# Optimization experiments

Hardware: AMD Instinct MI355X
Metric: run time of the kernel (lower is better)

The kernel has to match this reference:

```python
import jax, jax.numpy as jnp
import numpy as np

M, IN, H, OUT, B = 64, 64, 256, 1, 4096


def setup_inputs() -> dict:
    key = jax.random.key(0)
    ks = jax.random.split(key, 7)
    s1 = 1.0 / np.sqrt(IN)
    s2 = 1.0 / np.sqrt(H)
    return {
        "xs": jax.random.normal(ks[0], (M, B, IN), dtype=jnp.float32),
        "W1": jax.random.uniform(ks[1], (M, IN, H), minval=-s1, maxval=s1, dtype=jnp.float32),
        "b1": jax.random.uniform(ks[2], (M, H), minval=-s1, maxval=s1, dtype=jnp.float32),
        "W2": jax.random.uniform(ks[3], (M, H, H), minval=-s2, maxval=s2, dtype=jnp.float32),
        "b2": jax.random.uniform(ks[4], (M, H), minval=-s2, maxval=s2, dtype=jnp.float32),
        "W3": jax.random.uniform(ks[5], (M, H, OUT), minval=-s2, maxval=s2, dtype=jnp.float32),
        "b3": jax.random.uniform(ks[6], (M, OUT), minval=-s2, maxval=s2, dtype=jnp.float32),
    }


def reference(xs, W1, b1, W2, b2, W3, b3):
    # Batched over models: [M, B, in] x [M, in, h] -> [M, B, h]
    h1 = jax.nn.relu(jnp.einsum("mbi,mih->mbh", xs, W1) + b1[:, None, :])
    h2 = jax.nn.relu(jnp.einsum("mbh,mhk->mbk", h1, W2) + b2[:, None, :])
    out = jnp.einsum("mbh,mho->mbo", h2, W3) + b3[:, None, :]
    return out  # [M, B, out]
```

## Files before the change

### kernel.cpp

```cpp
#include <hip/hip_runtime.h>

#define NMODELS 64
#define BBATCH  4096
#define IN_DIM  64
#define H_DIM   256

typedef __attribute__((ext_vector_type(8))) short short8;
typedef __attribute__((ext_vector_type(4))) short short4v;
typedef __attribute__((ext_vector_type(4))) float floatx4;

__device__ __forceinline__ unsigned short f2bf(float f) {
    unsigned int u = __builtin_bit_cast(unsigned int, f);
    return (unsigned short)((u + 0x8000u) >> 16);
}

__global__ __launch_bounds__(256) void prep_weights(const float* __restrict__ W1,
                                                    const float* __restrict__ W2,
                                                    unsigned short* __restrict__ w1t,
                                                    unsigned short* __restrict__ w2t) {
    __shared__ float lds[64][65];
    const int bid = blockIdx.x;
    const float* src;
    unsigned short* dst;
    int K, N, m, kb, nb;
    if (bid < 256) {
        m = bid >> 2; kb = 0; nb = bid & 3; K = IN_DIM; N = H_DIM;
        src = W1; dst = w1t;
    } else {
        int t = bid - 256;
        m = t >> 4; kb = (t >> 2) & 3; nb = t & 3; K = H_DIM; N = H_DIM;
        src = W2; dst = w2t;
    }
    const float* s = src + ((size_t)m * K + (size_t)kb * 64) * N + nb * 64;
    const int tid = threadIdx.x;
    const int r = tid >> 4, c4 = (tid & 15) * 4;
#pragma unroll
    for (int p = 0; p < 4; ++p) {
        int row = p * 16 + r;
        float4 v = *(const float4*)(s + (size_t)row * N + c4);
        lds[row][c4] = v.x; lds[row][c4 + 1] = v.y;
        lds[row][c4 + 2] = v.z; lds[row][c4 + 3] = v.w;
    }
    __syncthreads();
    const int n = tid & 63, kg = tid >> 6;
    unsigned short tmp[16];
#pragma unroll
    for (int j = 0; j < 16; ++j) tmp[j] = f2bf(lds[kg * 16 + j][n]);
    unsigned short* d = dst + ((size_t)m * N + (size_t)(nb * 64 + n)) * K + kb * 64 + kg * 16;
    *(short8*)d = *(const short8*)tmp;
    *(short8*)(d + 8) = *(const short8*)(tmp + 8);
}

__global__ __launch_bounds__(256, 4) void mlp_fused(
    const float* __restrict__ xs,
    const unsigned short* __restrict__ w1t,
    const float* __restrict__ b1,
    const unsigned short* __restrict__ w2t,
    const float* __restrict__ b2,
    const float* __restrict__ w3,
    const float* __restrict__ b3,
    float* __restrict__ out)
{
    __shared__ unsigned short h1s[64 * 256];
    float* red = (float*)h1s;

    const int bid = blockIdx.x;
    const int m   = bid >> 6;
    const int tb  = bid & 63;
    const int tid = threadIdx.x;
    const int w   = tid >> 6;
    const int lane = tid & 63;
    const int q   = lane >> 4;
    const int c16 = lane & 15;
    const int sw  = c16 & 7;

    const float* xrow = xs + ((size_t)m * BBATCH + (size_t)tb * 64) * IN_DIM;
    const unsigned short* w1p = w1t + (size_t)m * (H_DIM * IN_DIM)
                                + (w * 64 + c16 * 4) * IN_DIM + q * 8;

    short8 ax[4][2];
#pragma unroll
    for (int rb = 0; rb < 4; ++rb)
#pragma unroll
        for (int kb = 0; kb < 2; ++kb) {
            const float* xp = xrow + (rb * 16 + c16) * IN_DIM + kb * 32 + q * 8;
            float4 v0 = *(const float4*)xp;
            float4 v1 = *(const float4*)(xp + 4);
            short8 a;
            a[0] = (short)f2bf(v0.x); a[1] = (short)f2bf(v0.y);
            a[2] = (short)f2bf(v0.z); a[3] = (short)f2bf(v0.w);
            a[4] = (short)f2bf(v1.x); a[5] = (short)f2bf(v1.y);
            a[6] = (short)f2bf(v1.z); a[7] = (short)f2bf(v1.w);
            ax[rb][kb] = a;
        }

    floatx4 acc[4][4];
#pragma unroll
    for (int rb = 0; rb < 4; ++rb)
#pragma unroll
        for (int nb = 0; nb < 4; ++nb)
            acc[rb][nb] = (floatx4){0.f, 0.f, 0.f, 0.f};

#pragma unroll
    for (int kb = 0; kb < 2; ++kb) {
        short8 bw[4];
#pragma unroll
        for (int nb = 0; nb < 4; ++nb)
            bw[nb] = *(const short8*)(w1p + nb * IN_DIM + kb * 32);
#pragma unroll
        for (int nb = 0; nb < 4; ++nb)
#pragma unroll
            for (int rb = 0; rb < 4; ++rb)
                acc[rb][nb] = __builtin_amdgcn_mfma_f32_16x16x32_bf16(
                    ax[rb][kb], bw[nb], acc[rb][nb], 0, 0, 0);
    }

    {
        floatx4 b1v = *(const floatx4*)(b1 + m * H_DIM + w * 64 + c16 * 4);
#pragma unroll
        for (int rb = 0; rb < 4; ++rb)
#pragma unroll
            for (int r = 0; r < 4; ++r) {
                short4v t;
#pragma unroll
                for (int nb = 0; nb < 4; ++nb)
                    t[nb] = (short)f2bf(fmaxf(acc[rb][nb][r] + b1v[nb], 0.f));
                int row = rb * 16 + q * 4 + r;
                int chunk = (w * 8 + (c16 >> 1)) ^ (row & 7);
                *(short4v*)((char*)h1s + row * 512 + chunk * 16 + (c16 & 1) * 8) = t;
            }
    }
    __syncthreads();

#pragma unroll
    for (int rb = 0; rb < 4; ++rb)
#pragma unroll
        for (int nb = 0; nb < 4; ++nb)
            acc[rb][nb] = (floatx4){0.f, 0.f, 0.f, 0.f};

    const unsigned short* w2p = w2t + (size_t)m * (H_DIM * H_DIM)
                                + (w * 64 + c16 * 4) * H_DIM + q * 8;
#pragma unroll
    for (int kb = 0; kb < 8; ++kb) {
        short8 av[4], bv[4];
#pragma unroll
        for (int rb = 0; rb < 4; ++rb)
            av[rb] = *(const short8*)((char*)h1s + (rb * 16 + c16) * 512
                                      + (((kb * 4 + q) ^ sw) * 16));
#pragma unroll
        for (int nb = 0; nb < 4; ++nb)
            bv[nb] = *(const short8*)(w2p + nb * H_DIM + kb * 32);
#pragma unroll
        for (int nb = 0; nb < 4; ++nb)
#pragma unroll
            for (int rb = 0; rb < 4; ++rb)
                acc[rb][nb] = __builtin_amdgcn_mfma_f32_16x16x32_bf16(
                    av[rb], bv[nb], acc[rb][nb], 0, 0, 0);
    }

    floatx4 b2v = *(const floatx4*)(b2 + m * H_DIM + w * 64 + c16 * 4);
    floatx4 w3v = *(const floatx4*)(w3 + m * H_DIM + w * 64 + c16 * 4);
    float p[4][4];
#pragma unroll
    for (int rb = 0; rb < 4; ++rb)
#pragma unroll
        for (int r = 0; r < 4; ++r) p[rb][r] = 0.f;
#pragma unroll
    for (int rb = 0; rb < 4; ++rb)
#pragma unroll
        for (int nb = 0; nb < 4; ++nb)
#pragma unroll
            for (int r = 0; r < 4; ++r) {
                float v = fmaxf(acc[rb][nb][r] + b2v[nb], 0.f);
                p[rb][r] += v * w3v[nb];
            }
#pragma unroll
    for (int off = 1; off < 16; off <<= 1)
#pragma unroll
        for (int rb = 0; rb < 4; ++rb)
#pragma unroll
            for (int r = 0; r < 4; ++r)
                p[rb][r] += __shfl_xor(p[rb][r], off);

    __syncthreads();
    if (c16 == 0) {
#pragma unroll
        for (int rb = 0; rb < 4; ++rb)
#pragma unroll
            for (int r = 0; r < 4; ++r)
                red[w * 64 + rb * 16 + q * 4 + r] = p[rb][r];
    }
    __syncthreads();
    if (tid < 64) {
        float s = red[tid] + red[64 + tid] + red[128 + tid] + red[192 + tid] + b3[m];
        out[(size_t)m * BBATCH + tb * 64 + tid] = s;
    }
}

extern "C" void kernel_launch(void* const* d_in, const int* in_sizes, int n_in,
                              void* d_out, int out_size, void* d_ws, size_t ws_size,
                              hipStream_t stream) {
    const float* xs = (const float*)d_in[0];
    const float* W1 = (const float*)d_in[1];
    const float* b1 = (const float*)d_in[2];
    const float* W2 = (const float*)d_in[3];
    const float* b2 = (const float*)d_in[4];
    const float* W3 = (const float*)d_in[5];
    const float* b3 = (const float*)d_in[6];
    float* out = (float*)d_out;

    unsigned short* w1t = (unsigned short*)d_ws;
    unsigned short* w2t = w1t + (size_t)NMODELS * H_DIM * IN_DIM;

    prep_weights<<<256 + NMODELS * 16, 256, 0, stream>>>(W1, W2, w1t, w2t);
    mlp_fused<<<NMODELS * (BBATCH / 64), 256, 0, stream>>>(xs, w1t, b1, w2t, b2, W3, b3, out);
}
```

Measured before the change: 208.5 us.

## Double-buffer W2 loads, replace shuffle reduction with LDS reduction, rework prep stores

The layer-2 loop now prefetches the next k-block of W2 fragments into a second register buffer while the MFMAs consume the current one, to hide global-load latency. The final 16-lane shuffle reduction is replaced by writing every partial to a padded LDS array, after which 64 threads each sum 64 values serially. The prep kernel's store pattern is reorganized so adjacent threads write contiguous 16-byte chunks along K. Launch bounds drop from 4 to 3 waves per SIMD, allowing more registers for the double buffer at the cost of lower occupancy. The serial 64-element tail sum adds latency on a single wave.

```diff
diff --git a/kernel.cpp b/kernel.cpp
--- a/kernel.cpp
+++ b/kernel.cpp
@@ -42,16 +42,19 @@
         lds[row][c4 + 2] = v.z; lds[row][c4 + 3] = v.w;
     }
     __syncthreads();
-    const int n = tid & 63, kg = tid >> 6;
-    unsigned short tmp[16];
-#pragma unroll
-    for (int j = 0; j < 16; ++j) tmp[j] = f2bf(lds[kg * 16 + j][n]);
-    unsigned short* d = dst + ((size_t)m * N + (size_t)(nb * 64 + n)) * K + kb * 64 + kg * 16;
-    *(short8*)d = *(const short8*)tmp;
-    *(short8*)(d + 8) = *(const short8*)(tmp + 8);
-}
-
-__global__ __launch_bounds__(256, 4) void mlp_fused(
+    unsigned short* dbase = dst + ((size_t)m * N + (size_t)nb * 64) * K + kb * 64;
+    const int j = tid & 7;
+#pragma unroll
+    for (int it = 0; it < 2; ++it) {
+        int n = it * 32 + (tid >> 3);
+        unsigned short tmp[8];
+#pragma unroll
+        for (int e = 0; e < 8; ++e) tmp[e] = f2bf(lds[j * 8 + e][n]);
+        *(short8*)(dbase + (size_t)n * K + j * 8) = *(const short8*)tmp;
+    }
+}
+
+__global__ __launch_bounds__(256, 3) void mlp_fused(
     const float* __restrict__ xs,
     const unsigned short* __restrict__ w1t,
     const float* __restrict__ b1,
@@ -140,22 +143,30 @@
 
     const unsigned short* w2p = w2t + (size_t)m * (H_DIM * H_DIM)
                                 + (w * 64 + c16 * 4) * H_DIM + q * 8;
+    short8 bvA[4], bvB[4];
+#pragma unroll
+    for (int nb = 0; nb < 4; ++nb)
+        bvA[nb] = *(const short8*)(w2p + nb * H_DIM);
 #pragma unroll
     for (int kb = 0; kb < 8; ++kb) {
-        short8 av[4], bv[4];
+        short8* cur = (kb & 1) ? bvB : bvA;
+        short8* nxt = (kb & 1) ? bvA : bvB;
+        if (kb < 7) {
+#pragma unroll
+            for (int nb = 0; nb < 4; ++nb)
+                nxt[nb] = *(const short8*)(w2p + nb * H_DIM + (kb + 1) * 32);
+        }
+        short8 av[4];
 #pragma unroll
         for (int rb = 0; rb < 4; ++rb)
             av[rb] = *(const short8*)((char*)h1s + (rb * 16 + c16) * 512
                                       + (((kb * 4 + q) ^ sw) * 16));
 #pragma unroll
         for (int nb = 0; nb < 4; ++nb)
-            bv[nb] = *(const short8*)(w2p + nb * H_DIM + kb * 32);
-#pragma unroll
-        for (int nb = 0; nb < 4; ++nb)
 #pragma unroll
             for (int rb = 0; rb < 4; ++rb)
                 acc[rb][nb] = __builtin_amdgcn_mfma_f32_16x16x32_bf16(
-                    av[rb], bv[nb], acc[rb][nb], 0, 0, 0);
+                    av[rb], cur[nb], acc[rb][nb], 0, 0, 0);
     }
 
     floatx4 b2v = *(const floatx4*)(b2 + m * H_DIM + w * 64 + c16 * 4);
@@ -174,25 +185,19 @@
                 float v = fmaxf(acc[rb][nb][r] + b2v[nb], 0.f);
                 p[rb][r] += v * w3v[nb];
             }
-#pragma unroll
-    for (int off = 1; off < 16; off <<= 1)
-#pragma unroll
-        for (int rb = 0; rb < 4; ++rb)
-#pragma unroll
-            for (int r = 0; r < 4; ++r)
-                p[rb][r] += __shfl_xor(p[rb][r], off);
-
-    __syncthreads();
-    if (c16 == 0) {
-#pragma unroll
-        for (int rb = 0; rb < 4; ++rb)
-#pragma unroll
-            for (int r = 0; r < 4; ++r)
-                red[w * 64 + rb * 16 + q * 4 + r] = p[rb][r];
-    }
+
+    __syncthreads();
+    const int unit = w * 16 + c16;
+#pragma unroll
+    for (int rb = 0; rb < 4; ++rb)
+#pragma unroll
+        for (int r = 0; r < 4; ++r)
+            red[(rb * 16 + q * 4 + r) * 65 + unit] = p[rb][r];
     __syncthreads();
     if (tid < 64) {
-        float s = red[tid] + red[64 + tid] + red[128 + tid] + red[192 + tid] + b3[m];
+        float s = b3[m];
+#pragma unroll
+        for (int u = 0; u < 64; ++u) s += red[tid * 65 + u];
         out[(size_t)m * BBATCH + tb * 64 + tid] = s;
     }
 }
```

New measurement: 212.4 us. No clear change (+1.9%).
